# Optimization experiments

Measured on AMD Instinct MI355X. Metric: run time of the kernel, lower is better.

The kernel has to match this reference:

```python
import jax, jax.numpy as jnp
import numpy as np

N = 4096      # nodes
FEAT = 512    # feature_size
HID = 256     # hidden_dim
E = 131072    # edges (avg degree 32)


def setup_inputs() -> dict:
    key = jax.random.key(0)
    ks = jax.random.split(key, 10)
    x = jax.random.normal(ks[0], (N, FEAT), dtype=jnp.float32)
    edge_index = jax.random.randint(ks[1], (2, E), 0, N)
    edge_attr = jax.random.uniform(ks[2], (E, 1), dtype=jnp.float32)
    # nn.Linear(bias=False) weights, stored as [in, out] so k = x @ Wk
    Wk = jax.random.normal(ks[3], (FEAT, HID), dtype=jnp.float32) / np.sqrt(FEAT)
    Wq = jax.random.normal(ks[4], (FEAT, HID), dtype=jnp.float32) / np.sqrt(FEAT)
    Wv = jax.random.normal(ks[5], (FEAT, FEAT), dtype=jnp.float32) / np.sqrt(FEAT)
    # EmbeddingTable.reset_parameters: normal(0, 1), shape [num_embeddings=2, dim]
    Ek = jax.random.normal(ks[6], (2, HID), dtype=jnp.float32)
    Eq = jax.random.normal(ks[7], (2, HID), dtype=jnp.float32)
    Ev = jax.random.normal(ks[8], (2, FEAT), dtype=jnp.float32)
    # ContinuousEmbeddingIndex params
    idx_bias = jnp.full((1,), 0.5, dtype=jnp.float32)
    idx_mult = jnp.full((1,), 10.0, dtype=jnp.float32)
    return dict(x=x, edge_index=edge_index, edge_attr=edge_attr,
                Wk=Wk, Wq=Wq, Wv=Wv, Ek=Ek, Eq=Eq, Ev=Ev,
                idx_bias=idx_bias, idx_mult=idx_mult)


def reference(x, edge_index, edge_attr, Wk, Wq, Wv, Ek, Eq, Ev, idx_bias, idx_mult):
    n = x.shape[0]
    L = x.shape[-1]  # feature_size, used as softmax scale
    src, dst = edge_index[0], edge_index[1]

    # ContinuousEmbeddingIndex: soft 2-way interpolation weights [E, 2]
    s = jax.nn.sigmoid((edge_attr - idx_bias) * idx_mult)
    w = jnp.concatenate([s, 1.0 - s], axis=-1)

    # per-edge relative embeddings (EmbeddingTable: weights @ embeddings)
    rk = w @ Ek   # [E, HID]
    rq = w @ Eq   # [E, HID]
    rv = w @ Ev   # [E, FEAT]

    k = x @ Wk    # [N, HID]
    q = x @ Wq    # [N, HID]
    v = x @ Wv    # [N, FEAT]

    # A = q k^T + (q_i . Rk_ij) + (k_j . Rq_ij) + q k^T
    # The Rk/Rq terms are nonzero only on edges -> compute per-edge and scatter-add
    # (to_dense_adj sums duplicate edges, matched by .add).
    A = 2.0 * (q @ k.T)                                   # [N, N]
    edge_bias = jnp.sum(q[src] * rk, axis=-1) + jnp.sum(k[dst] * rq, axis=-1)  # [E]
    A = A.at[src, dst].add(edge_bias)
    A = jax.nn.softmax(A / np.sqrt(L), axis=-1)           # dropout = identity (eval)

    # M = A v + sum_j A_ij * Rv_ij  (second term only nonzero on edges)
    M = A @ v
    M = M + jax.ops.segment_sum(A[src, dst][:, None] * rv, src, num_segments=n)
    return M
```

## Files before the change

kernel.cpp:

```cpp
#include <hip/hip_runtime.h>
#include <hip/hip_bf16.h>
#include <cmath>


typedef short bf16x8 __attribute__((ext_vector_type(8)));
typedef float f32x4  __attribute__((ext_vector_type(4)));
typedef unsigned short ushort_t;
typedef unsigned short ushort4v __attribute__((ext_vector_type(4)));
typedef unsigned short ushort8v __attribute__((ext_vector_type(8)));

__device__ __forceinline__ ushort_t f2bf(float f) {
    union { float f; unsigned u; } v; v.f = f;
    unsigned u = v.u;
    u += 0x7FFFu + ((u >> 16) & 1u);
    return (ushort_t)(u >> 16);
}
__device__ __forceinline__ float bf2f(ushort_t h) {
    union { unsigned u; float f; } v; v.u = ((unsigned)h) << 16;
    return v.f;
}
__device__ __forceinline__ void gload_lds16(const void* g, void* l) {
    __builtin_amdgcn_global_load_lds(
        (const __attribute__((address_space(1))) void*)g,
        (__attribute__((address_space(3))) void*)l, 16, 0, 0);
}

template<bool STORE_BF16>
__device__ __forceinline__ void gemm_body_nt(
    const ushort_t* __restrict__ A, const ushort_t* __restrict__ B,
    void* __restrict__ Cv, int lda, int ldb, int ldc, int Ksz, float alpha,
    int bm, int bn, size_t kbase, ushort_t* As, ushort_t* Bs)
{
    constexpr int BK = 32;
    const int tid  = threadIdx.x;
    const int lane = tid & 63;
    const int wid  = tid >> 6;
    const int wm = (wid >> 1) * 64;
    const int wn = (wid & 1) * 64;

    f32x4 acc[4][4] = {};

    const int r0 = tid >> 2;
    const int c8 = (tid & 3) * 8;
    const ushort_t* Ag0 = A + (size_t)(bm + r0) * lda + kbase + c8;
    const ushort_t* Bg0 = B + (size_t)(bn + r0) * ldb + kbase + c8;
    const ushort_t* Ag1 = Ag0 + (size_t)64 * lda;
    const ushort_t* Bg1 = Bg0 + (size_t)64 * ldb;
    ushort_t* AsW0 = &As[(wid * 64) * 8];
    ushort_t* AsW1 = &As[(256 + wid * 64) * 8];
    ushort_t* BsW0 = &Bs[(wid * 64) * 8];
    ushort_t* BsW1 = &Bs[(256 + wid * 64) * 8];

    const int fr = lane & 15;
    const int kh = (lane >> 4) * 8;

    for (int k0 = 0; k0 < Ksz; k0 += BK) {
        gload_lds16(Ag0 + k0, AsW0);
        gload_lds16(Ag1 + k0, AsW1);
        gload_lds16(Bg0 + k0, BsW0);
        gload_lds16(Bg1 + k0, BsW1);
        __syncthreads();

        bf16x8 af[4], bfv[4];
        #pragma unroll
        for (int i = 0; i < 4; ++i) {
            af[i]  = *(const bf16x8*)&As[(wm + i * 16 + fr) * 32 + kh];
            bfv[i] = *(const bf16x8*)&Bs[(wn + i * 16 + fr) * 32 + kh];
        }
        #pragma unroll
        for (int i = 0; i < 4; ++i)
            #pragma unroll
            for (int j = 0; j < 4; ++j)
                acc[i][j] = __builtin_amdgcn_mfma_f32_16x16x32_bf16(
                    af[i], bfv[j], acc[i][j], 0, 0, 0);
        __syncthreads();
    }

    const int cr = (lane >> 4) * 4;
    const int cc = lane & 15;
    #pragma unroll
    for (int i = 0; i < 4; ++i)
        #pragma unroll
        for (int j = 0; j < 4; ++j) {
            const int col = bn + wn + j * 16 + cc;
            const int rowb = bm + wm + i * 16 + cr;
            #pragma unroll
            for (int jj = 0; jj < 4; ++jj) {
                const float val = alpha * acc[i][j][jj];
                if (STORE_BF16)
                    ((ushort_t*)Cv)[(size_t)(rowb + jj) * ldc + col] = f2bf(val);
                else
                    ((float*)Cv)[(size_t)(rowb + jj) * ldc + col] = val;
            }
        }
}

template<bool STORE_BF16>
__global__ __launch_bounds__(256) void gemm_nt_mfma(
    const ushort_t* __restrict__ A, const ushort_t* __restrict__ B,
    void* __restrict__ Cv, int lda, int ldb, int ldc,
    int Ksz, float alpha, size_t zstride)
{
    __shared__ ushort_t As[128 * 32];
    __shared__ ushort_t Bs[128 * 32];

    int bid = blockIdx.y * gridDim.x + blockIdx.x;
    const int nwg = gridDim.x * gridDim.y;
    if ((nwg & 7) == 0) {
        const int cpx = nwg >> 3;
        bid = (bid & 7) * cpx + (bid >> 3);
    }
    const int bm = (bid / gridDim.x) * 128;
    const int bn = (bid % gridDim.x) * 128;
    const size_t kbase = (size_t)blockIdx.z * Ksz;
    void* Cz = STORE_BF16 ? Cv : (void*)((float*)Cv + (size_t)blockIdx.z * zstride);
    gemm_body_nt<STORE_BF16>(A, B, Cz, lda, ldb, ldc, Ksz, alpha, bm, bn, kbase, As, Bs);
}

__global__ __launch_bounds__(256) void proj_gemm(
    const ushort_t* __restrict__ xb, const ushort_t* __restrict__ Wqkt,
    const ushort_t* __restrict__ Wvt, ushort_t* __restrict__ qkb,
    ushort_t* __restrict__ vTb, int FEAT, int HID, int N)
{
    __shared__ ushort_t As[128 * 32];
    __shared__ ushort_t Bs[128 * 32];
    const int b = blockIdx.x;
    if (b < 128) {
        const int gx = (2 * HID) / 128;
        const int bm = (b / gx) * 128, bn = (b % gx) * 128;
        gemm_body_nt<true>(xb, Wqkt, qkb, FEAT, FEAT, 2 * HID, FEAT, 1.f,
                           bm, bn, 0, As, Bs);
    } else {
        const int b2 = b - 128;
        const int gx = N / 128;
        const int bm = (b2 / gx) * 128, bn = (b2 % gx) * 128;
        gemm_body_nt<true>(Wvt, xb, vTb, FEAT, FEAT, N, FEAT, 1.f,
                           bm, bn, 0, As, Bs);
    }
}

__global__ __launch_bounds__(256) void prep_kernel(
    const float* __restrict__ x, const float* __restrict__ Wq,
    const float* __restrict__ Wk, const float* __restrict__ Wv,
    ushort_t* __restrict__ xb, ushort_t* __restrict__ Wqkt,
    ushort_t* __restrict__ Wvt, int N, int FEAT, int HID)
{
    const int xBlocks = (N * FEAT / 8) / 256;
    const int wBlocks = (HID * FEAT) / 256;
    const int b = blockIdx.x;
    if (b < xBlocks) {
        const int i = b * 256 + threadIdx.x;
        const float4 a = ((const float4*)x)[2 * i];
        const float4 c = ((const float4*)x)[2 * i + 1];
        ushort8v o;
        o[0] = f2bf(a.x); o[1] = f2bf(a.y); o[2] = f2bf(a.z); o[3] = f2bf(a.w);
        o[4] = f2bf(c.x); o[5] = f2bf(c.y); o[6] = f2bf(c.z); o[7] = f2bf(c.w);
        ((ushort8v*)xb)[i] = o;
    } else if (b < xBlocks + wBlocks) {
        const int idx = (b - xBlocks) * 256 + threadIdx.x;
        const int o = idx / FEAT, i = idx % FEAT;
        Wqkt[idx] = f2bf(Wq[(size_t)i * HID + o]);
    } else if (b < xBlocks + 2 * wBlocks) {
        const int idx = (b - xBlocks - wBlocks) * 256 + threadIdx.x;
        const int o = idx / FEAT, i = idx % FEAT;
        Wqkt[(size_t)HID * FEAT + idx] = f2bf(Wk[(size_t)i * HID + o]);
    } else {
        const int idx = (b - xBlocks - 2 * wBlocks) * 256 + threadIdx.x;
        const int o = idx / FEAT, i = idx % FEAT;
        Wvt[idx] = f2bf(Wv[(size_t)i * FEAT + o]);
    }
}

__global__ __launch_bounds__(256) void node_dots(
    const ushort_t* __restrict__ qk,
    const float* __restrict__ Ek, const float* __restrict__ Eq,
    float* qk0, float* qk1, float* kq0, float* kq1,
    float* c0, float* c1, int HID)
{
    const int node = blockIdx.x;
    const int t = threadIdx.x;
    const ushort_t* row = qk + (size_t)node * (2 * HID);
    const float qv = bf2f(row[t]);
    const float kv = bf2f(row[HID + t]);
    float p0 = qv * Ek[t];
    float p1 = qv * Ek[HID + t];
    float p2 = kv * Eq[t];
    float p3 = kv * Eq[HID + t];
    #pragma unroll
    for (int off = 32; off > 0; off >>= 1) {
        p0 += __shfl_down(p0, off);
        p1 += __shfl_down(p1, off);
        p2 += __shfl_down(p2, off);
        p3 += __shfl_down(p3, off);
    }
    __shared__ float red[4][4];
    if ((t & 63) == 0) {
        const int w = t >> 6;
        red[w][0] = p0; red[w][1] = p1; red[w][2] = p2; red[w][3] = p3;
    }
    __syncthreads();
    if (t == 0) {
        qk0[node] = red[0][0] + red[1][0] + red[2][0] + red[3][0];
        qk1[node] = red[0][1] + red[1][1] + red[2][1] + red[3][1];
        kq0[node] = red[0][2] + red[1][2] + red[2][2] + red[3][2];
        kq1[node] = red[0][3] + red[1][3] + red[2][3] + red[3][3];
        c0[node] = 0.f;
        c1[node] = 0.f;
    }
}

__global__ void edge_bias_kernel(
    const int* __restrict__ ei, const float* __restrict__ attr,
    const float* __restrict__ qk0, const float* __restrict__ qk1,
    const float* __restrict__ kq0, const float* __restrict__ kq1,
    float* __restrict__ A, int E, int N,
    const float* __restrict__ ibp, const float* __restrict__ imp)
{
    const int e = blockIdx.x * blockDim.x + threadIdx.x;
    if (e >= E) return;
    const int src = ei[e];
    const int dst = ei[E + e];
    const float s = 1.f / (1.f + __expf(-(attr[e] - ibp[0]) * imp[0]));
    const float bias = s * qk0[src] + (1.f - s) * qk1[src]
                     + s * kq0[dst] + (1.f - s) * kq1[dst];
    atomicAdd(&A[(size_t)src * N + dst], bias);
}

__global__ __launch_bounds__(256) void softmax_rows_bf16(
    const float* __restrict__ A, ushort_t* __restrict__ P, int N, float scale)
{
    const int row = blockIdx.x;
    const float* a = A + (size_t)row * N;
    ushort_t* p = P + (size_t)row * N;
    const int t = threadIdx.x;
    float4 vals[4];
    float mx = -1e30f;
    #pragma unroll
    for (int u = 0; u < 4; ++u) {
        float4 vv = ((const float4*)a)[t + u * 256];
        vv.x *= scale; vv.y *= scale; vv.z *= scale; vv.w *= scale;
        vals[u] = vv;
        mx = fmaxf(mx, fmaxf(fmaxf(vv.x, vv.y), fmaxf(vv.z, vv.w)));
    }
    __shared__ float red[4];
    #pragma unroll
    for (int off = 32; off > 0; off >>= 1) mx = fmaxf(mx, __shfl_down(mx, off));
    if ((t & 63) == 0) red[t >> 6] = mx;
    __syncthreads();
    const float m = fmaxf(fmaxf(red[0], red[1]), fmaxf(red[2], red[3]));
    __syncthreads();
    float sum = 0.f;
    #pragma unroll
    for (int u = 0; u < 4; ++u) {
        vals[u].x = __expf(vals[u].x - m);
        vals[u].y = __expf(vals[u].y - m);
        vals[u].z = __expf(vals[u].z - m);
        vals[u].w = __expf(vals[u].w - m);
        sum += vals[u].x + vals[u].y + vals[u].z + vals[u].w;
    }
    #pragma unroll
    for (int off = 32; off > 0; off >>= 1) sum += __shfl_down(sum, off);
    if ((t & 63) == 0) red[t >> 6] = sum;
    __syncthreads();
    const float inv = 1.f / (red[0] + red[1] + red[2] + red[3]);
    #pragma unroll
    for (int u = 0; u < 4; ++u) {
        ushort4v o;
        o[0] = f2bf(vals[u].x * inv);
        o[1] = f2bf(vals[u].y * inv);
        o[2] = f2bf(vals[u].z * inv);
        o[3] = f2bf(vals[u].w * inv);
        ((ushort4v*)p)[t + u * 256] = o;
    }
}

__global__ void edge_coeff_kernel(
    const int* __restrict__ ei, const float* __restrict__ attr,
    const ushort_t* __restrict__ P, float* __restrict__ c0, float* __restrict__ c1,
    int E, int N, const float* __restrict__ ibp, const float* __restrict__ imp)
{
    const int e = blockIdx.x * blockDim.x + threadIdx.x;
    if (e >= E) return;
    const int src = ei[e];
    const int dst = ei[E + e];
    const float s = 1.f / (1.f + __expf(-(attr[e] - ibp[0]) * imp[0]));
    const float pv = bf2f(P[(size_t)src * N + dst]);
    atomicAdd(&c0[src], pv * s);
    atomicAdd(&c1[src], pv * (1.f - s));
}

__global__ void reduce_add_rv_kernel(
    const float* __restrict__ parts, float* __restrict__ out,
    const float* __restrict__ c0, const float* __restrict__ c1,
    const float* __restrict__ Ev, int FEAT, size_t zstride, int nz)
{
    const int i4 = blockIdx.x * 256 + threadIdx.x;
    const int F4 = FEAT / 4;
    const int node = i4 / F4;
    const int f4 = i4 % F4;
    float4 acc = ((const float4*)parts)[i4];
    for (int z = 1; z < nz; ++z) {
        const float4 p = *(const float4*)(parts + (size_t)z * zstride + (size_t)i4 * 4);
        acc.x += p.x; acc.y += p.y; acc.z += p.z; acc.w += p.w;
    }
    const float a0 = c0[node], a1 = c1[node];
    const float4 e0 = ((const float4*)Ev)[f4];
    const float4 e1 = ((const float4*)Ev)[F4 + f4];
    acc.x += a0 * e0.x + a1 * e1.x;
    acc.y += a0 * e0.y + a1 * e1.y;
    acc.z += a0 * e0.z + a1 * e1.z;
    acc.w += a0 * e0.w + a1 * e1.w;
    ((float4*)out)[i4] = acc;
}

extern "C" void kernel_launch(void* const* d_in, const int* in_sizes, int n_in,
                              void* d_out, int out_size, void* d_ws, size_t ws_size,
                              hipStream_t stream)
{
    const float* x    = (const float*)d_in[0];
    const int*   ei   = (const int*)d_in[1];
    const float* attr = (const float*)d_in[2];
    const float* Wk   = (const float*)d_in[3];
    const float* Wq   = (const float*)d_in[4];
    const float* Wv   = (const float*)d_in[5];
    const float* Ek   = (const float*)d_in[6];
    const float* Eq   = (const float*)d_in[7];
    const float* Ev   = (const float*)d_in[8];
    const float* ib   = (const float*)d_in[9];
    const float* im   = (const float*)d_in[10];
    float* out = (float*)d_out;

    const int FEAT = (int)lroundf(sqrtf((float)in_sizes[5]));
    const int HID  = in_sizes[3] / FEAT;
    const int N    = in_sizes[0] / FEAT;
    const int E    = in_sizes[2];

    char* w = (char*)d_ws;
    size_t o = 0;
    ushort_t* xb   = (ushort_t*)(w + o); o += (size_t)N * FEAT * 2;
    ushort_t* Wqkt = (ushort_t*)(w + o); o += (size_t)2 * HID * FEAT * 2;
    ushort_t* Wvt  = (ushort_t*)(w + o); o += (size_t)FEAT * FEAT * 2;
    ushort_t* qkb  = (ushort_t*)(w + o); o += (size_t)N * 2 * HID * 2;
    ushort_t* vTb  = (ushort_t*)(w + o); o += (size_t)FEAT * N * 2;
    float*    Abuf = (float*)(w + o);    o += (size_t)N * N * 4;
    ushort_t* Pb   = (ushort_t*)(w + o); o += (size_t)N * N * 2;
    float*    qk0  = (float*)(w + o);    o += (size_t)N * 4;
    float*    qk1  = (float*)(w + o);    o += (size_t)N * 4;
    float*    kq0  = (float*)(w + o);    o += (size_t)N * 4;
    float*    kq1  = (float*)(w + o);    o += (size_t)N * 4;
    float*    c0   = (float*)(w + o);    o += (size_t)N * 4;
    float*    c1   = (float*)(w + o);    o += (size_t)N * 4;
    float*    pvpart = Abuf;

    const dim3 blk(256);
    const int NZ = 4;
    const int Kchunk = N / NZ;

    const int prepBlocks = (N * FEAT / 8) / 256 + 2 * ((HID * FEAT) / 256)
                         + (FEAT * FEAT) / 256;
    prep_kernel<<<prepBlocks, blk, 0, stream>>>(x, Wq, Wk, Wv, xb, Wqkt, Wvt,
                                                N, FEAT, HID);

    proj_gemm<<<256, blk, 0, stream>>>(xb, Wqkt, Wvt, qkb, vTb, FEAT, HID, N);

    node_dots<<<N, blk, 0, stream>>>(qkb, Ek, Eq, qk0, qk1, kq0, kq1, c0, c1, HID);

    gemm_nt_mfma<false><<<dim3(N / 128, N / 128), blk, 0, stream>>>(
        qkb, qkb + HID, Abuf, 2 * HID, 2 * HID, N, HID, 2.f, 0);

    edge_bias_kernel<<<(E + 255) / 256, blk, 0, stream>>>(ei, attr, qk0, qk1, kq0, kq1,
                                                          Abuf, E, N, ib, im);

    softmax_rows_bf16<<<N, blk, 0, stream>>>(Abuf, Pb, N, 1.f / sqrtf((float)FEAT));

    edge_coeff_kernel<<<(E + 255) / 256, blk, 0, stream>>>(ei, attr, Pb, c0, c1, E, N, ib, im);

    gemm_nt_mfma<false><<<dim3(FEAT / 128, N / 128, NZ), blk, 0, stream>>>(
        Pb, vTb, pvpart, N, N, FEAT, Kchunk, 1.f, (size_t)N * FEAT);

    reduce_add_rv_kernel<<<(N * FEAT / 4 + 255) / 256, blk, 0, stream>>>(
        pvpart, out, c0, c1, Ev, FEAT, (size_t)N * FEAT, NZ);
}
```

Measured before the change: 132.7 us.

## Replace split-K partial buffers with atomic accumulation and 256x128 PV tiles

The P·V GEMM no longer writes four split-K partial buffers that a separate reduction kernel sums. Instead, a small init kernel writes the Rv edge term into the output, and a new 512-thread GEMM with 256x128 tiles atomically adds each split-K slice into it. This removes the partial-buffer write and read traffic and the reduction pass, and the larger tile reuses each V load across more rows. In exchange it adds heavy float atomic traffic and makes the summation order nondeterministic. The new kernel also has no double buffering.

```diff
diff --git a/kernel.cpp b/kernel.cpp
--- a/kernel.cpp
+++ b/kernel.cpp
@@ -98,8 +98,7 @@
 template<bool STORE_BF16>
 __global__ __launch_bounds__(256) void gemm_nt_mfma(
     const ushort_t* __restrict__ A, const ushort_t* __restrict__ B,
-    void* __restrict__ Cv, int lda, int ldb, int ldc,
-    int Ksz, float alpha, size_t zstride)
+    void* __restrict__ Cv, int lda, int ldb, int ldc, int Ksz, float alpha)
 {
     __shared__ ushort_t As[128 * 32];
     __shared__ ushort_t Bs[128 * 32];
@@ -112,9 +111,7 @@
     }
     const int bm = (bid / gridDim.x) * 128;
     const int bn = (bid % gridDim.x) * 128;
-    const size_t kbase = (size_t)blockIdx.z * Ksz;
-    void* Cz = STORE_BF16 ? Cv : (void*)((float*)Cv + (size_t)blockIdx.z * zstride);
-    gemm_body_nt<STORE_BF16>(A, B, Cz, lda, ldb, ldc, Ksz, alpha, bm, bn, kbase, As, Bs);
+    gemm_body_nt<STORE_BF16>(A, B, Cv, lda, ldb, ldc, Ksz, alpha, bm, bn, 0, As, Bs);
 }
 
 __global__ __launch_bounds__(256) void proj_gemm(
@@ -137,6 +134,99 @@
         gemm_body_nt<true>(Wvt, xb, vTb, FEAT, FEAT, N, FEAT, 1.f,
                            bm, bn, 0, As, Bs);
     }
+}
+
+__global__ __launch_bounds__(512) void pv_gemm_atomic(
+    const ushort_t* __restrict__ P, const ushort_t* __restrict__ vT,
+    float* __restrict__ out, int N, int FEAT, int Kchunk)
+{
+    constexpr int BK = 32;
+    __shared__ ushort_t As[256 * BK];
+    __shared__ ushort_t Bs[128 * BK];
+
+    int bid = blockIdx.y * gridDim.x + blockIdx.x;
+    const int nwg = gridDim.x * gridDim.y;
+    if ((nwg & 7) == 0) {
+        const int cpx = nwg >> 3;
+        bid = (bid & 7) * cpx + (bid >> 3);
+    }
+    const int bm = (bid / gridDim.x) * 256;
+    const int bn = (bid % gridDim.x) * 128;
+
+    const int tid  = threadIdx.x;
+    const int lane = tid & 63;
+    const int wid  = tid >> 6;
+    const int wm = (wid >> 1) * 64;
+    const int wn = (wid & 1) * 64;
+
+    f32x4 acc[4][4] = {};
+
+    const size_t kbase = (size_t)blockIdx.z * Kchunk;
+    const int r0 = tid >> 2;
+    const int c8 = (tid & 3) * 8;
+    const ushort_t* Ag0 = P  + (size_t)(bm + r0) * N + kbase + c8;
+    const ushort_t* Ag1 = Ag0 + (size_t)128 * N;
+    const ushort_t* Bg0 = vT + (size_t)(bn + r0) * N + kbase + c8;
+    ushort_t* AsW0 = &As[wid * 512];
+    ushort_t* AsW1 = &As[4096 + wid * 512];
+    ushort_t* BsW0 = &Bs[wid * 512];
+
+    const int fr = lane & 15;
+    const int kh = (lane >> 4) * 8;
+
+    for (int k0 = 0; k0 < Kchunk; k0 += BK) {
+        gload_lds16(Ag0 + k0, AsW0);
+        gload_lds16(Ag1 + k0, AsW1);
+        gload_lds16(Bg0 + k0, BsW0);
+        __syncthreads();
+
+        bf16x8 af[4], bfv[4];
+        #pragma unroll
+        for (int i = 0; i < 4; ++i) {
+            af[i]  = *(const bf16x8*)&As[(wm + i * 16 + fr) * 32 + kh];
+            bfv[i] = *(const bf16x8*)&Bs[(wn + i * 16 + fr) * 32 + kh];
+        }
+        #pragma unroll
+        for (int i = 0; i < 4; ++i)
+            #pragma unroll
+            for (int j = 0; j < 4; ++j)
+                acc[i][j] = __builtin_amdgcn_mfma_f32_16x16x32_bf16(
+                    af[i], bfv[j], acc[i][j], 0, 0, 0);
+        __syncthreads();
+    }
+
+    const int cr = (lane >> 4) * 4;
+    const int cc = lane & 15;
+    #pragma unroll
+    for (int i = 0; i < 4; ++i) {
+        const int rowb = bm + wm + i * 16 + cr;
+        #pragma unroll
+        for (int j = 0; j < 4; ++j) {
+            const int col = bn + wn + j * 16 + cc;
+            #pragma unroll
+            for (int jj = 0; jj < 4; ++jj)
+                atomicAdd(&out[(size_t)(rowb + jj) * FEAT + col], acc[i][j][jj]);
+        }
+    }
+}
+
+__global__ void init_out_kernel(
+    float* __restrict__ out, const float* __restrict__ c0,
+    const float* __restrict__ c1, const float* __restrict__ Ev, int FEAT)
+{
+    const int i4 = blockIdx.x * 256 + threadIdx.x;
+    const int F4 = FEAT / 4;
+    const int node = i4 / F4;
+    const int f4 = i4 % F4;
+    const float a0 = c0[node], a1 = c1[node];
+    const float4 e0 = ((const float4*)Ev)[f4];
+    const float4 e1 = ((const float4*)Ev)[F4 + f4];
+    float4 o;
+    o.x = a0 * e0.x + a1 * e1.x;
+    o.y = a0 * e0.y + a1 * e1.y;
+    o.z = a0 * e0.z + a1 * e1.z;
+    o.w = a0 * e0.w + a1 * e1.w;
+    ((float4*)out)[i4] = o;
 }
 
 __global__ __launch_bounds__(256) void prep_kernel(
@@ -289,30 +379,6 @@
     atomicAdd(&c1[src], pv * (1.f - s));
 }
 
-__global__ void reduce_add_rv_kernel(
-    const float* __restrict__ parts, float* __restrict__ out,
-    const float* __restrict__ c0, const float* __restrict__ c1,
-    const float* __restrict__ Ev, int FEAT, size_t zstride, int nz)
-{
-    const int i4 = blockIdx.x * 256 + threadIdx.x;
-    const int F4 = FEAT / 4;
-    const int node = i4 / F4;
-    const int f4 = i4 % F4;
-    float4 acc = ((const float4*)parts)[i4];
-    for (int z = 1; z < nz; ++z) {
-        const float4 p = *(const float4*)(parts + (size_t)z * zstride + (size_t)i4 * 4);
-        acc.x += p.x; acc.y += p.y; acc.z += p.z; acc.w += p.w;
-    }
-    const float a0 = c0[node], a1 = c1[node];
-    const float4 e0 = ((const float4*)Ev)[f4];
-    const float4 e1 = ((const float4*)Ev)[F4 + f4];
-    acc.x += a0 * e0.x + a1 * e1.x;
-    acc.y += a0 * e0.y + a1 * e1.y;
-    acc.z += a0 * e0.z + a1 * e1.z;
-    acc.w += a0 * e0.w + a1 * e1.w;
-    ((float4*)out)[i4] = acc;
-}
-
 extern "C" void kernel_launch(void* const* d_in, const int* in_sizes, int n_in,
                               void* d_out, int out_size, void* d_ws, size_t ws_size,
                               hipStream_t stream)
@@ -350,7 +416,6 @@
     float*    kq1  = (float*)(w + o);    o += (size_t)N * 4;
     float*    c0   = (float*)(w + o);    o += (size_t)N * 4;
     float*    c1   = (float*)(w + o);    o += (size_t)N * 4;
-    float*    pvpart = Abuf;
 
     const dim3 blk(256);
     const int NZ = 4;
@@ -366,7 +431,7 @@
     node_dots<<<N, blk, 0, stream>>>(qkb, Ek, Eq, qk0, qk1, kq0, kq1, c0, c1, HID);
 
     gemm_nt_mfma<false><<<dim3(N / 128, N / 128), blk, 0, stream>>>(
-        qkb, qkb + HID, Abuf, 2 * HID, 2 * HID, N, HID, 2.f, 0);
+        qkb, qkb + HID, Abuf, 2 * HID, 2 * HID, N, HID, 2.f);
 
     edge_bias_kernel<<<(E + 255) / 256, blk, 0, stream>>>(ei, attr, qk0, qk1, kq0, kq1,
                                                           Abuf, E, N, ib, im);
@@ -375,9 +440,8 @@
 
     edge_coeff_kernel<<<(E + 255) / 256, blk, 0, stream>>>(ei, attr, Pb, c0, c1, E, N, ib, im);
 
-    gemm_nt_mfma<false><<<dim3(FEAT / 128, N / 128, NZ), blk, 0, stream>>>(
-        Pb, vTb, pvpart, N, N, FEAT, Kchunk, 1.f, (size_t)N * FEAT);
-
-    reduce_add_rv_kernel<<<(N * FEAT / 4 + 255) / 256, blk, 0, stream>>>(
-        pvpart, out, c0, c1, Ev, FEAT, (size_t)N * FEAT, NZ);
-}
+    init_out_kernel<<<(N * FEAT / 4) / 256, blk, 0, stream>>>(out, c0, c1, Ev, FEAT);
+
+    pv_gemm_atomic<<<dim3(FEAT / 128, N / 256, NZ), dim3(512), 0, stream>>>(
+        Pb, vTb, out, N, FEAT, Kchunk);
+}
```

After: 150.7 us. 13.5% more time.

## Fuse split-K reduction into PV GEMM and tile weight transposes

Applied to the files above, without the earlier changes.

The separate split-K reduce kernel is replaced by a ticket counter per output tile. The last-arriving split-K block sums the partials and adds the Rv edge term directly, which removes one kernel launch and one full pass over the partial buffers from a separate kernel. The weight transpose in prep now goes through a 32x32 shared-memory tile to coalesce both reads and writes. The cost is atomics, threadfences and a serial reduction tail inside the GEMM blocks, plus counters that are reset in the prep kernel.

```diff
diff --git a/kernel.cpp b/kernel.cpp
--- a/kernel.cpp
+++ b/kernel.cpp
@@ -25,11 +25,10 @@
         (__attribute__((address_space(3))) void*)l, 16, 0, 0);
 }
 
-template<bool STORE_BF16>
-__device__ __forceinline__ void gemm_body_nt(
+__device__ __forceinline__ void gemm_core(
     const ushort_t* __restrict__ A, const ushort_t* __restrict__ B,
-    void* __restrict__ Cv, int lda, int ldb, int ldc, int Ksz, float alpha,
-    int bm, int bn, size_t kbase, ushort_t* As, ushort_t* Bs)
+    int lda, int ldb, int Ksz, size_t kbase, int bm, int bn,
+    ushort_t* As, ushort_t* Bs, f32x4 (&acc)[4][4])
 {
     constexpr int BK = 32;
     const int tid  = threadIdx.x;
@@ -37,8 +36,6 @@
     const int wid  = tid >> 6;
     const int wm = (wid >> 1) * 64;
     const int wn = (wid & 1) * 64;
-
-    f32x4 acc[4][4] = {};
 
     const int r0 = tid >> 2;
     const int c8 = (tid & 3) * 8;
@@ -75,9 +72,36 @@
                     af[i], bfv[j], acc[i][j], 0, 0, 0);
         __syncthreads();
     }
-
-    const int cr = (lane >> 4) * 4;
-    const int cc = lane & 15;
+}
+
+__device__ __forceinline__ int swizzle_bid()
+{
+    int bid = blockIdx.y * gridDim.x + blockIdx.x;
+    const int nwg = gridDim.x * gridDim.y;
+    if ((nwg & 7) == 0) {
+        const int cpx = nwg >> 3;
+        bid = (bid & 7) * cpx + (bid >> 3);
+    }
+    return bid;
+}
+
+template<bool STORE_BF16>
+__global__ __launch_bounds__(256) void gemm_nt_mfma(
+    const ushort_t* __restrict__ A, const ushort_t* __restrict__ B,
+    void* __restrict__ Cv, int lda, int ldb, int ldc, int Ksz, float alpha)
+{
+    __shared__ ushort_t As[128 * 32];
+    __shared__ ushort_t Bs[128 * 32];
+    const int bid = swizzle_bid();
+    const int bm = (bid / gridDim.x) * 128;
+    const int bn = (bid % gridDim.x) * 128;
+    f32x4 acc[4][4] = {};
+    gemm_core(A, B, lda, ldb, Ksz, 0, bm, bn, As, Bs, acc);
+
+    const int lane = threadIdx.x & 63;
+    const int wid  = threadIdx.x >> 6;
+    const int wm = (wid >> 1) * 64, wn = (wid & 1) * 64;
+    const int cr = (lane >> 4) * 4, cc = lane & 15;
     #pragma unroll
     for (int i = 0; i < 4; ++i)
         #pragma unroll
@@ -95,28 +119,6 @@
         }
 }
 
-template<bool STORE_BF16>
-__global__ __launch_bounds__(256) void gemm_nt_mfma(
-    const ushort_t* __restrict__ A, const ushort_t* __restrict__ B,
-    void* __restrict__ Cv, int lda, int ldb, int ldc,
-    int Ksz, float alpha, size_t zstride)
-{
-    __shared__ ushort_t As[128 * 32];
-    __shared__ ushort_t Bs[128 * 32];
-
-    int bid = blockIdx.y * gridDim.x + blockIdx.x;
-    const int nwg = gridDim.x * gridDim.y;
-    if ((nwg & 7) == 0) {
-        const int cpx = nwg >> 3;
-        bid = (bid & 7) * cpx + (bid >> 3);
-    }
-    const int bm = (bid / gridDim.x) * 128;
-    const int bn = (bid % gridDim.x) * 128;
-    const size_t kbase = (size_t)blockIdx.z * Ksz;
-    void* Cz = STORE_BF16 ? Cv : (void*)((float*)Cv + (size_t)blockIdx.z * zstride);
-    gemm_body_nt<STORE_BF16>(A, B, Cz, lda, ldb, ldc, Ksz, alpha, bm, bn, kbase, As, Bs);
-}
-
 __global__ __launch_bounds__(256) void proj_gemm(
     const ushort_t* __restrict__ xb, const ushort_t* __restrict__ Wqkt,
     const ushort_t* __restrict__ Wvt, ushort_t* __restrict__ qkb,
@@ -125,17 +127,98 @@
     __shared__ ushort_t As[128 * 32];
     __shared__ ushort_t Bs[128 * 32];
     const int b = blockIdx.x;
+    const ushort_t* A; const ushort_t* B; ushort_t* C;
+    int bm, bn, ldc;
     if (b < 128) {
         const int gx = (2 * HID) / 128;
-        const int bm = (b / gx) * 128, bn = (b % gx) * 128;
-        gemm_body_nt<true>(xb, Wqkt, qkb, FEAT, FEAT, 2 * HID, FEAT, 1.f,
-                           bm, bn, 0, As, Bs);
+        bm = (b / gx) * 128; bn = (b % gx) * 128;
+        A = xb; B = Wqkt; C = qkb; ldc = 2 * HID;
     } else {
         const int b2 = b - 128;
         const int gx = N / 128;
-        const int bm = (b2 / gx) * 128, bn = (b2 % gx) * 128;
-        gemm_body_nt<true>(Wvt, xb, vTb, FEAT, FEAT, N, FEAT, 1.f,
-                           bm, bn, 0, As, Bs);
+        bm = (b2 / gx) * 128; bn = (b2 % gx) * 128;
+        A = Wvt; B = xb; C = vTb; ldc = N;
+    }
+    f32x4 acc[4][4] = {};
+    gemm_core(A, B, FEAT, FEAT, FEAT, 0, bm, bn, As, Bs, acc);
+
+    const int lane = threadIdx.x & 63;
+    const int wid  = threadIdx.x >> 6;
+    const int wm = (wid >> 1) * 64, wn = (wid & 1) * 64;
+    const int cr = (lane >> 4) * 4, cc = lane & 15;
+    #pragma unroll
+    for (int i = 0; i < 4; ++i)
+        #pragma unroll
+        for (int j = 0; j < 4; ++j) {
+            const int col = bn + wn + j * 16 + cc;
+            const int rowb = bm + wm + i * 16 + cr;
+            #pragma unroll
+            for (int jj = 0; jj < 4; ++jj)
+                C[(size_t)(rowb + jj) * ldc + col] = f2bf(acc[i][j][jj]);
+        }
+}
+
+__global__ __launch_bounds__(256) void pv_gemm_splitk(
+    const ushort_t* __restrict__ P, const ushort_t* __restrict__ vT,
+    float* __restrict__ parts, float* __restrict__ out,
+    const float* __restrict__ c0, const float* __restrict__ c1,
+    const float* __restrict__ Ev, int* __restrict__ counters,
+    int N, int FEAT, int Kchunk, int NZ)
+{
+    __shared__ ushort_t As[128 * 32];
+    __shared__ ushort_t Bs[128 * 32];
+    const int bid = swizzle_bid();
+    const int bm = (bid / gridDim.x) * 128;
+    const int bn = (bid % gridDim.x) * 128;
+    const size_t zs = (size_t)N * FEAT;
+
+    f32x4 acc[4][4] = {};
+    gemm_core(P, vT, N, N, Kchunk, (size_t)blockIdx.z * Kchunk, bm, bn, As, Bs, acc);
+
+    const int tid = threadIdx.x;
+    const int lane = tid & 63;
+    const int wid  = tid >> 6;
+    const int wm = (wid >> 1) * 64, wn = (wid & 1) * 64;
+    const int cr = (lane >> 4) * 4, cc = lane & 15;
+    float* myPart = parts + (size_t)blockIdx.z * zs;
+    #pragma unroll
+    for (int i = 0; i < 4; ++i)
+        #pragma unroll
+        for (int j = 0; j < 4; ++j) {
+            const int col = bn + wn + j * 16 + cc;
+            const int rowb = bm + wm + i * 16 + cr;
+            #pragma unroll
+            for (int jj = 0; jj < 4; ++jj)
+                myPart[(size_t)(rowb + jj) * FEAT + col] = acc[i][j][jj];
+        }
+
+    __threadfence();
+    const int tileid = (bm >> 7) * gridDim.x + (bn >> 7);
+    __shared__ int ticket;
+    if (tid == 0) ticket = atomicAdd(&counters[tileid], 1);
+    __syncthreads();
+    if (ticket != NZ - 1) return;
+    __threadfence();
+
+    const int r  = bm + (tid >> 1);
+    const int cb = bn + (tid & 1) * 64;
+    const float a0 = c0[r], a1 = c1[r];
+    #pragma unroll 4
+    for (int c4 = 0; c4 < 16; ++c4) {
+        const int col = cb + c4 * 4;
+        const size_t off = (size_t)r * FEAT + col;
+        float4 s = *(const float4*)(parts + off);
+        for (int z = 1; z < NZ; ++z) {
+            const float4 p = *(const float4*)(parts + (size_t)z * zs + off);
+            s.x += p.x; s.y += p.y; s.z += p.z; s.w += p.w;
+        }
+        const float4 e0 = *(const float4*)(Ev + col);
+        const float4 e1 = *(const float4*)(Ev + FEAT + col);
+        s.x += a0 * e0.x + a1 * e1.x;
+        s.y += a0 * e0.y + a1 * e1.y;
+        s.z += a0 * e0.z + a1 * e1.z;
+        s.w += a0 * e0.w + a1 * e1.w;
+        *(float4*)(out + off) = s;
     }
 }
 
@@ -143,32 +226,44 @@
     const float* __restrict__ x, const float* __restrict__ Wq,
     const float* __restrict__ Wk, const float* __restrict__ Wv,
     ushort_t* __restrict__ xb, ushort_t* __restrict__ Wqkt,
-    ushort_t* __restrict__ Wvt, int N, int FEAT, int HID)
-{
+    ushort_t* __restrict__ Wvt, int* __restrict__ counters,
+    int N, int FEAT, int HID)
+{
+    const int b = blockIdx.x;
+    const int tid = threadIdx.x;
+    if (b == 0 && tid < 128) counters[tid] = 0;
+
     const int xBlocks = (N * FEAT / 8) / 256;
-    const int wBlocks = (HID * FEAT) / 256;
-    const int b = blockIdx.x;
     if (b < xBlocks) {
-        const int i = b * 256 + threadIdx.x;
+        const int i = b * 256 + tid;
         const float4 a = ((const float4*)x)[2 * i];
         const float4 c = ((const float4*)x)[2 * i + 1];
         ushort8v o;
         o[0] = f2bf(a.x); o[1] = f2bf(a.y); o[2] = f2bf(a.z); o[3] = f2bf(a.w);
         o[4] = f2bf(c.x); o[5] = f2bf(c.y); o[6] = f2bf(c.z); o[7] = f2bf(c.w);
         ((ushort8v*)xb)[i] = o;
-    } else if (b < xBlocks + wBlocks) {
-        const int idx = (b - xBlocks) * 256 + threadIdx.x;
-        const int o = idx / FEAT, i = idx % FEAT;
-        Wqkt[idx] = f2bf(Wq[(size_t)i * HID + o]);
-    } else if (b < xBlocks + 2 * wBlocks) {
-        const int idx = (b - xBlocks - wBlocks) * 256 + threadIdx.x;
-        const int o = idx / FEAT, i = idx % FEAT;
-        Wqkt[(size_t)HID * FEAT + idx] = f2bf(Wk[(size_t)i * HID + o]);
-    } else {
-        const int idx = (b - xBlocks - 2 * wBlocks) * 256 + threadIdx.x;
-        const int o = idx / FEAT, i = idx % FEAT;
-        Wvt[idx] = f2bf(Wv[(size_t)i * FEAT + o]);
-    }
+        return;
+    }
+
+    __shared__ float tile[32][33];
+    const int qkTiles = (FEAT / 32) * (HID / 32);
+    int t = b - xBlocks;
+    const float* src; ushort_t* dst; int I, O;
+    if (t < qkTiles)            { src = Wq; dst = Wqkt;                       I = FEAT; O = HID; }
+    else if (t < 2 * qkTiles)   { src = Wk; dst = Wqkt + (size_t)HID * FEAT;  I = FEAT; O = HID; t -= qkTiles; }
+    else                        { src = Wv; dst = Wvt;                        I = FEAT; O = FEAT; t -= 2 * qkTiles; }
+    const int ot = O / 32;
+    const int r0 = (t / ot) * 32;
+    const int c0 = (t % ot) * 32;
+    const int lr = tid >> 5;
+    const int lc = tid & 31;
+    #pragma unroll
+    for (int rr = 0; rr < 32; rr += 8)
+        tile[lr + rr][lc] = src[(size_t)(r0 + lr + rr) * O + c0 + lc];
+    __syncthreads();
+    #pragma unroll
+    for (int rr = 0; rr < 32; rr += 8)
+        dst[(size_t)(c0 + lr + rr) * I + r0 + lc] = f2bf(tile[lc][lr + rr]);
 }
 
 __global__ __launch_bounds__(256) void node_dots(
@@ -287,30 +382,6 @@
     const float pv = bf2f(P[(size_t)src * N + dst]);
     atomicAdd(&c0[src], pv * s);
     atomicAdd(&c1[src], pv * (1.f - s));
-}
-
-__global__ void reduce_add_rv_kernel(
-    const float* __restrict__ parts, float* __restrict__ out,
-    const float* __restrict__ c0, const float* __restrict__ c1,
-    const float* __restrict__ Ev, int FEAT, size_t zstride, int nz)
-{
-    const int i4 = blockIdx.x * 256 + threadIdx.x;
-    const int F4 = FEAT / 4;
-    const int node = i4 / F4;
-    const int f4 = i4 % F4;
-    float4 acc = ((const float4*)parts)[i4];
-    for (int z = 1; z < nz; ++z) {
-        const float4 p = *(const float4*)(parts + (size_t)z * zstride + (size_t)i4 * 4);
-        acc.x += p.x; acc.y += p.y; acc.z += p.z; acc.w += p.w;
-    }
-    const float a0 = c0[node], a1 = c1[node];
-    const float4 e0 = ((const float4*)Ev)[f4];
-    const float4 e1 = ((const float4*)Ev)[F4 + f4];
-    acc.x += a0 * e0.x + a1 * e1.x;
-    acc.y += a0 * e0.y + a1 * e1.y;
-    acc.z += a0 * e0.z + a1 * e1.z;
-    acc.w += a0 * e0.w + a1 * e1.w;
-    ((float4*)out)[i4] = acc;
 }
 
 extern "C" void kernel_launch(void* const* d_in, const int* in_sizes, int n_in,
@@ -350,23 +421,25 @@
     float*    kq1  = (float*)(w + o);    o += (size_t)N * 4;
     float*    c0   = (float*)(w + o);    o += (size_t)N * 4;
     float*    c1   = (float*)(w + o);    o += (size_t)N * 4;
+    int*      cnt  = (int*)(w + o);      o += 128 * 4;
     float*    pvpart = Abuf;
 
     const dim3 blk(256);
     const int NZ = 4;
     const int Kchunk = N / NZ;
 
-    const int prepBlocks = (N * FEAT / 8) / 256 + 2 * ((HID * FEAT) / 256)
-                         + (FEAT * FEAT) / 256;
-    prep_kernel<<<prepBlocks, blk, 0, stream>>>(x, Wq, Wk, Wv, xb, Wqkt, Wvt,
-                                                N, FEAT, HID);
+    const int xBlocks = (N * FEAT / 8) / 256;
+    const int qkTiles = (FEAT / 32) * (HID / 32);
+    const int vTiles  = (FEAT / 32) * (FEAT / 32);
+    prep_kernel<<<xBlocks + 2 * qkTiles + vTiles, blk, 0, stream>>>(
+        x, Wq, Wk, Wv, xb, Wqkt, Wvt, cnt, N, FEAT, HID);
 
     proj_gemm<<<256, blk, 0, stream>>>(xb, Wqkt, Wvt, qkb, vTb, FEAT, HID, N);
 
     node_dots<<<N, blk, 0, stream>>>(qkb, Ek, Eq, qk0, qk1, kq0, kq1, c0, c1, HID);
 
     gemm_nt_mfma<false><<<dim3(N / 128, N / 128), blk, 0, stream>>>(
-        qkb, qkb + HID, Abuf, 2 * HID, 2 * HID, N, HID, 2.f, 0);
+        qkb, qkb + HID, Abuf, 2 * HID, 2 * HID, N, HID, 2.f);
 
     edge_bias_kernel<<<(E + 255) / 256, blk, 0, stream>>>(ei, attr, qk0, qk1, kq0, kq1,
                                                           Abuf, E, N, ib, im);
@@ -375,9 +448,6 @@
 
     edge_coeff_kernel<<<(E + 255) / 256, blk, 0, stream>>>(ei, attr, Pb, c0, c1, E, N, ib, im);
 
-    gemm_nt_mfma<false><<<dim3(FEAT / 128, N / 128, NZ), blk, 0, stream>>>(
-        Pb, vTb, pvpart, N, N, FEAT, Kchunk, 1.f, (size_t)N * FEAT);
-
-    reduce_add_rv_kernel<<<(N * FEAT / 4 + 255) / 256, blk, 0, stream>>>(
-        pvpart, out, c0, c1, Ev, FEAT, (size_t)N * FEAT, NZ);
-}
+    pv_gemm_splitk<<<dim3(FEAT / 128, N / 128, NZ), blk, 0, stream>>>(
+        Pb, vTb, pvpart, out, c0, c1, Ev, cnt, N, FEAT, Kchunk, NZ);
+}
```

New measurement: 218.9 us. 64.9% more time.
